# Optimization experiments

Measured on AMD Instinct MI355X. Metric: run time of the kernel, lower is better.

## Reference

```python
import jax, jax.numpy as jnp
import numpy as np
import math

B, S, HID = 2, 2048, 1152
NH, NKV = 16, 4
HD = HID // NH  # 72
GROUPS = NH // NKV  # 4
ROPE_BASE = 10000.0


def setup_inputs() -> dict:
    key = jax.random.key(0)
    ks = jax.random.split(key, 5)
    hidden_states = jax.random.normal(ks[0], (B, S, HID), dtype=jnp.float32)
    # causal additive mask: 0 on/below diagonal, -1e9 above
    causal = jnp.tril(jnp.ones((S, S), dtype=jnp.bool_))
    attention_mask = jnp.where(causal, 0.0, -1e9).astype(jnp.float32)[None, None]
    scale = 0.02
    wq = jax.random.normal(ks[1], (HID, HID), dtype=jnp.float32) * scale
    wk = jax.random.normal(ks[2], (NKV * HD, HID), dtype=jnp.float32) * scale
    wv = jax.random.normal(ks[3], (NKV * HD, HID), dtype=jnp.float32) * scale
    wo = jax.random.normal(ks[4], (HID, HID), dtype=jnp.float32) * scale
    return {"hidden_states": hidden_states, "attention_mask": attention_mask,
            "wq": wq, "wk": wk, "wv": wv, "wo": wo}


def _rotate_half(x):
    x1, x2 = jnp.split(x, 2, axis=-1)
    return jnp.concatenate((-x2, x1), axis=-1)


def _rope_cos_sin(seq_len, dim, dtype):
    inv_freq = 1.0 / (ROPE_BASE ** (jnp.arange(0, dim, 2, dtype=jnp.float32) / dim))
    t = jnp.arange(seq_len, dtype=jnp.float32)
    freqs = jnp.outer(t, inv_freq)          # [S, dim/2]
    emb = jnp.concatenate((freqs, freqs), axis=-1)  # [S, dim]
    return jnp.cos(emb).astype(dtype), jnp.sin(emb).astype(dtype)


def reference(hidden_states, attention_mask, wq, wk, wv, wo):
    b, s, _ = hidden_states.shape
    # projections (nn.Linear: x @ W.T)
    q = (hidden_states @ wq.T).reshape(b, s, NH, HD).transpose(0, 2, 1, 3)    # [b,nh,s,hd]
    k = (hidden_states @ wk.T).reshape(b, s, NKV, HD).transpose(0, 2, 1, 3)   # [b,nkv,s,hd]
    v = (hidden_states @ wv.T).reshape(b, s, NKV, HD).transpose(0, 2, 1, 3)
    # RoPE
    cos, sin = _rope_cos_sin(s, HD, hidden_states.dtype)
    cos, sin = cos[None, None], sin[None, None]  # [1,1,s,hd]
    q = q * cos + _rotate_half(q) * sin
    k = k * cos + _rotate_half(k) * sin
    # expand kv heads (repeat_interleave over head dim)
    k = jnp.repeat(k, GROUPS, axis=1)  # [b,nh,s,hd]
    v = jnp.repeat(v, GROUPS, axis=1)
    scores = jnp.einsum('bhqd,bhkd->bhqk', q, k) / math.sqrt(HD)
    scores = scores + attention_mask
    attn = jax.nn.softmax(scores.astype(jnp.float32), axis=-1).astype(q.dtype)
    out = jnp.einsum('bhqk,bhkd->bhqd', attn, v)
    out = out.transpose(0, 2, 1, 3).reshape(b, s, HID)
    return out @ wo.T
```

## Files before the change

### kernel.cpp

```cpp
#include <hip/hip_runtime.h>
#include <hip/hip_bf16.h>
#include <cstddef>

#define B_   2
#define S_   2048
#define HID_ 1152
#define NH_  16
#define NKV_ 4
#define HD_  72
#define MTOT (B_ * S_)
#define KVDIM (NKV_ * HD_)

typedef float f32x4 __attribute__((ext_vector_type(4)));
typedef short bf16x8 __attribute__((ext_vector_type(8)));
typedef short s4v __attribute__((ext_vector_type(4)));

__device__ __forceinline__ float bf2f(short x) {
  unsigned int u = ((unsigned int)(unsigned short)x) << 16;
  return __builtin_bit_cast(float, u);
}
__device__ __forceinline__ short f2bf(float f) {
  unsigned int u = __builtin_bit_cast(unsigned int, f);
  u += 0x7fff + ((u >> 16) & 1);
  return (short)(u >> 16);
}

__device__ __forceinline__ float fast_exp2(float x) {
#if __has_builtin(__builtin_amdgcn_exp2f)
  return __builtin_amdgcn_exp2f(x);
#else
  return exp2f(x);
#endif
}

__device__ __forceinline__ void async16(const short* g, short* lds) {
  __builtin_amdgcn_global_load_lds((const __attribute__((address_space(1))) void*)g,
                                   (__attribute__((address_space(3))) void*)lds,
                                   16, 0, 0);
}

__global__ void k_cvt_all(const float4* __restrict__ s0, const float4* __restrict__ s1,
                          const float4* __restrict__ s2, const float4* __restrict__ s3,
                          const float4* __restrict__ s4,
                          s4v* __restrict__ d0, s4v* __restrict__ d1, s4v* __restrict__ d2,
                          s4v* __restrict__ d3, s4v* __restrict__ d4,
                          float2* __restrict__ tab,
                          int n0, int n1, int n2, int n3, int n4t) {
  int ncvt = n0 + n1 + n2 + n3 + n4t;
  int total = ncvt + S_ * 36;
  for (int i = blockIdx.x * blockDim.x + threadIdx.x; i < total;
       i += gridDim.x * blockDim.x) {
    if (i < ncvt) {
      const float4* s;
      s4v* d;
      int off = i;
      if (off < n0) { s = s0; d = d0; }
      else {
        off -= n0;
        if (off < n1) { s = s1; d = d1; }
        else {
          off -= n1;
          if (off < n2) { s = s2; d = d2; }
          else {
            off -= n2;
            if (off < n3) { s = s3; d = d3; }
            else { off -= n3; s = s4; d = d4; }
          }
        }
      }
      float4 v = s[off];
      s4v o = { f2bf(v.x), f2bf(v.y), f2bf(v.z), f2bf(v.w) };
      d[off] = o;
    } else {
      int idx = i - ncvt;
      int ii = idx % 36, s = idx / 36;
      float freq = powf(10000.0f, -(float)ii / 36.0f);
      float a = (float)s * freq;
      tab[idx] = make_float2(cosf(a), sinf(a));
    }
  }
}

__global__ void k_post(short* __restrict__ Qb, short* __restrict__ Kb,
                       const short* __restrict__ Vb, short* __restrict__ Vt,
                       const float2* __restrict__ tab) {
  int idx = blockIdx.x * blockDim.x + threadIdx.x;
  const int nrope = MTOT * 20 * 36;
  if (idx < nrope) {
    int i = idx % 36;
    int t = idx / 36;
    int hh = t % 20;
    int m = t / 20;
    int s = m & (S_ - 1);
    float2 cs = tab[s * 36 + i];
    short* p = (hh < 16) ? Qb + (size_t)m * HID_ + hh * HD_
                         : Kb + (size_t)m * KVDIM + (hh - 16) * HD_;
    float x1 = bf2f(p[i]), x2 = bf2f(p[i + 36]);
    p[i]      = f2bf(x1 * cs.x - x2 * cs.y);
    p[i + 36] = f2bf(x2 * cs.x + x1 * cs.y);
  } else {
    idx -= nrope;
    if (idx >= 8 * 80 * S_) return;
    int s = idx & (S_ - 1);
    int t2 = idx >> 11;
    int d = t2 % 80;
    int bkv = t2 / 80;
    int b = bkv >> 2, kv = bkv & 3;
    short v = 0;
    if (d < HD_) v = Vb[((size_t)(b * S_ + s)) * KVDIM + kv * HD_ + d];
    else if (d == HD_) v = (short)0x3F80;
    Vt[idx] = v;
  }
}

#define BM 128
#define BN 128
#define BK 32

__global__ __launch_bounds__(256) void k_gemm_qkv(const short* __restrict__ A,
                                                  const short* __restrict__ Wq,
                                                  const short* __restrict__ Wk,
                                                  const short* __restrict__ Wv,
                                                  short* __restrict__ Qo,
                                                  short* __restrict__ Ko,
                                                  short* __restrict__ Vo) {
  const int K = HID_, NTOT = 1728;
  __shared__ short As[BM * BK];
  __shared__ short Bs[BN * BK];
  const int tid = threadIdx.x;
  const int l = tid & 63;
  const int w = tid >> 6;
  const int bm = blockIdx.x * BM;
  const int bn = blockIdx.y * BN;
  const int wr = (w >> 1) * 64;
  const int wc = (w & 1) * 64;
  const int c15 = l & 15, g = l >> 4;
  const int r0 = tid >> 2;
  const int c0 = (tid & 3) * 8;

  f32x4 acc[4][4] = {};

  for (int k0 = 0; k0 < K; k0 += BK) {
#pragma unroll
    for (int it = 0; it < 2; ++it) {
      int ar = bm + it * 64 + r0;
      int br = bn + it * 64 + r0;
      if (br > NTOT - 1) br = NTOT - 1;
      const short* bsrc;
      if (br < 1152)      bsrc = Wq + (size_t)br * K;
      else if (br < 1440) bsrc = Wk + (size_t)(br - 1152) * K;
      else                bsrc = Wv + (size_t)(br - 1440) * K;
      async16(A + (size_t)ar * K + k0 + c0, &As[(it * 64 + r0) * BK + c0]);
      async16(bsrc + k0 + c0, &Bs[(it * 64 + r0) * BK + c0]);
    }
    __syncthreads();
    bf16x8 af[4], bfr[4];
#pragma unroll
    for (int t = 0; t < 4; ++t) {
      af[t]  = *(const bf16x8*)&As[(wr + t * 16 + c15) * BK + g * 8];
      bfr[t] = *(const bf16x8*)&Bs[(wc + t * 16 + c15) * BK + g * 8];
    }
#pragma unroll
    for (int mt = 0; mt < 4; ++mt)
#pragma unroll
      for (int nt = 0; nt < 4; ++nt)
        acc[mt][nt] = __builtin_amdgcn_mfma_f32_16x16x32_bf16(af[mt], bfr[nt], acc[mt][nt], 0, 0, 0);
    __syncthreads();
  }

#pragma unroll
  for (int mt = 0; mt < 4; ++mt)
#pragma unroll
    for (int nt = 0; nt < 4; ++nt)
#pragma unroll
      for (int j = 0; j < 4; ++j) {
        int row = bm + wr + mt * 16 + g * 4 + j;
        int col = bn + wc + nt * 16 + c15;
        short val = f2bf(acc[mt][nt][j]);
        if (col < 1152)      Qo[(size_t)row * HID_ + col] = val;
        else if (col < 1440) Ko[(size_t)row * KVDIM + col - 1152] = val;
        else if (col < NTOT) Vo[(size_t)row * KVDIM + col - 1440] = val;
      }
}

__global__ __launch_bounds__(256) void k_gemm_o(const short* __restrict__ A,
                                                const short* __restrict__ Bm,
                                                float* __restrict__ C,
                                                int M, int N, int K) {
  __shared__ short As[BM * BK];
  __shared__ short Bs[BN * BK];
  const int tid = threadIdx.x;
  const int l = tid & 63;
  const int w = tid >> 6;
  const int bm = blockIdx.x * BM;
  const int bn = blockIdx.y * BN;
  const int wr = (w >> 1) * 64;
  const int wc = (w & 1) * 64;
  const int c15 = l & 15, g = l >> 4;
  const int r0 = tid >> 2;
  const int c0 = (tid & 3) * 8;

  f32x4 acc[4][4] = {};

  for (int k0 = 0; k0 < K; k0 += BK) {
#pragma unroll
    for (int it = 0; it < 2; ++it) {
      int ar = bm + it * 64 + r0;
      int br = bn + it * 64 + r0;
      if (br > N - 1) br = N - 1;
      async16(A + (size_t)ar * K + k0 + c0, &As[(it * 64 + r0) * BK + c0]);
      async16(Bm + (size_t)br * K + k0 + c0, &Bs[(it * 64 + r0) * BK + c0]);
    }
    __syncthreads();
    bf16x8 af[4], bfr[4];
#pragma unroll
    for (int t = 0; t < 4; ++t) {
      af[t]  = *(const bf16x8*)&As[(wr + t * 16 + c15) * BK + g * 8];
      bfr[t] = *(const bf16x8*)&Bs[(wc + t * 16 + c15) * BK + g * 8];
    }
#pragma unroll
    for (int mt = 0; mt < 4; ++mt)
#pragma unroll
      for (int nt = 0; nt < 4; ++nt)
        acc[mt][nt] = __builtin_amdgcn_mfma_f32_16x16x32_bf16(af[mt], bfr[nt], acc[mt][nt], 0, 0, 0);
    __syncthreads();
  }

#pragma unroll
  for (int mt = 0; mt < 4; ++mt)
#pragma unroll
    for (int nt = 0; nt < 4; ++nt)
#pragma unroll
      for (int j = 0; j < 4; ++j) {
        int row = bm + wr + mt * 16 + g * 4 + j;
        int col = bn + wc + nt * 16 + c15;
        if (col < N) C[(size_t)row * N + col] = acc[mt][nt][j];
      }
}

#define QB 16
#define KT 64

__global__ __launch_bounds__(256, 2) void k_flash(const short* __restrict__ Q,
                                                  const short* __restrict__ Kg,
                                                  const short* __restrict__ Vt,
                                                  short* __restrict__ O) {
  const int bid = blockIdx.x;
  const int bkv = bid & 7;
  const int qt = 127 - (bid >> 3);
  const int b = bkv >> 2, kv = bkv & 3;
  const int tid = threadIdx.x;
  const int w = tid >> 6, l = tid & 63;
  const int h = kv * 4 + w;
  const int q0 = qt * QB;
  const int c15 = l & 15, g = l >> 4;

  __shared__ short lds[24064];
  short* Ks0 = lds;
  short* Ks1 = lds + 9728;
  short* Ps  = lds + 19456 + w * 1152;

  const float SCL = 0.117851130f * 1.4426950408889634f;
  const float SHIFT = 8.0f;

  const short* Qbase = Q + (size_t)(b * S_) * HID_ + h * HD_;
  const short* Kbase = Kg + (size_t)(b * S_) * KVDIM + kv * HD_;
  const short* Vbase = Vt + (size_t)bkv * 80 * S_;

  const short* gk[3];
  const short* gv[3];
  int lk[3], lv[3];
  bool vkf[3], vvf[3];
#pragma unroll
  for (int i = 0; i < 3; ++i) {
    int c = tid + 256 * i;
    vkf[i] = c < 576;
    int row = c / 9, cc = c - row * 9;
    if (row > 63) row = 63;
    gk[i] = Kbase + (size_t)row * KVDIM + cc * 8;
    lk[i] = c < 576 ? c * 8 : 0;
    int c2 = tid + 256 * i;
    vvf[i] = c2 < 640;
    int vrow = (c2 >> 3) & 127, slot = c2 & 7;
    if (vrow > 79) vrow = 79;
    gv[i] = Vbase + (size_t)vrow * S_ + ((slot ^ (vrow & 7)) << 3);
    lv[i] = c2 < 640 ? c2 * 8 : 0;
  }

  const int lane_k = c15 * 72 + g * 8;
  const short* rKa = Ks0 + lane_k;
  const short* rKb = Ks1 + lane_k;
  const int lane_v0 = 4608 + c15 * 64 + ((g ^ (c15 & 7)) << 3);
  const int lane_v1 = 4608 + c15 * 64 + (((4 + g) ^ (c15 & 7)) << 3);
  const short* rV0a = lds + lane_v0;
  const short* rV0b = lds + 9728 + lane_v0;
  const short* rV1a = lds + lane_v1;
  const short* rV1b = lds + 9728 + lane_v1;
  short* pPw = Ps + g * 288 + c15;
  const short* pPr = Ps + c15 * 72 + g * 8;

  bf16x8 qf[3];
  const bf16x8 zfrag = {0, 0, 0, 0, 0, 0, 0, 0};
  {
    int row = q0 + c15;
#pragma unroll
    for (int ks = 0; ks < 3; ++ks) {
      int d0 = ks * 32 + g * 8;
      qf[ks] = (d0 < HD_) ? *(const bf16x8*)(Qbase + (size_t)row * HID_ + d0) : zfrag;
    }
#pragma unroll
    for (int ks = 0; ks < 3; ++ks)
#pragma unroll
      for (int e = 0; e < 8; ++e)
        qf[ks][e] = f2bf(bf2f(qf[ks][e]) * SCL);
  }

  f32x4 accO[5] = {};

  const int nkt = (q0 + QB + KT - 1) / KT;
  const int nfull = (QB * qt + 1) >> 6;

  auto STAGE = [&](short* Kd, short* Vd) {
#pragma unroll
    for (int i = 0; i < 3; ++i) {
      if (vkf[i]) async16(gk[i], Kd + lk[i]);
      if (vvf[i]) async16(gv[i], Vd + lv[i]);
      gk[i] += KT * KVDIM;
      gv[i] += KT;
    }
  };

  STAGE(Ks0, lds + 4608);
  const short *rKc = rKa, *rKn = rKb;
  const short *rV0c = rV0a, *rV0n = rV0b;
  const short *rV1c = rV1a, *rV1n = rV1b;
  short *sKn = Ks1, *sVn = lds + 14336;
  short *sKc = Ks0, *sVc = lds + 4608;

  for (int kt = 0; kt < nkt; ++kt) {
    asm volatile("s_waitcnt vmcnt(0)" ::: "memory");
    __builtin_amdgcn_sched_barrier(0);
    __syncthreads();
    if (kt + 1 < nkt) STAGE(sKn, sVn);

    const int kbase = kt * KT;

    f32x4 sc[4] = {};
    __builtin_amdgcn_s_setprio(1);
#pragma unroll
    for (int ct = 0; ct < 4; ++ct)
#pragma unroll
      for (int ks = 0; ks < 3; ++ks) {
        bf16x8 kf = *(const bf16x8*)&rKc[ct * 1152 + ks * 32];
        sc[ct] = __builtin_amdgcn_mfma_f32_16x16x32_bf16(qf[ks], kf, sc[ct], 0, 0, 0);
      }
    __builtin_amdgcn_s_setprio(0);

    const int qrow = q0 + g * 4;
    if (kt >= nfull) {
#pragma unroll
      for (int ct = 0; ct < 4; ++ct) {
        int col = kbase + ct * 16 + c15;
#pragma unroll
        for (int j = 0; j < 4; ++j)
          if (col > qrow + j) sc[ct][j] = -1e30f;
      }
    }
#pragma unroll
    for (int ct = 0; ct < 4; ++ct)
#pragma unroll
      for (int j = 0; j < 4; ++j)
        sc[ct][j] = fast_exp2(sc[ct][j] - SHIFT);

#pragma unroll
    for (int ct = 0; ct < 4; ++ct)
#pragma unroll
      for (int j = 0; j < 4; ++j)
        pPw[j * 72 + ct * 16] = f2bf(sc[ct][j]);
    asm volatile("s_waitcnt lgkmcnt(0)" ::: "memory");
    __builtin_amdgcn_sched_barrier(0);
    bf16x8 pa0 = *(const bf16x8*)&pPr[0];
    bf16x8 pa1 = *(const bf16x8*)&pPr[32];

    __builtin_amdgcn_s_setprio(1);
#pragma unroll
    for (int dt = 0; dt < 5; ++dt) {
      bf16x8 vb0 = *(const bf16x8*)&rV0c[dt * 1024];
      bf16x8 vb1 = *(const bf16x8*)&rV1c[dt * 1024];
      accO[dt] = __builtin_amdgcn_mfma_f32_16x16x32_bf16(pa0, vb0, accO[dt], 0, 0, 0);
      accO[dt] = __builtin_amdgcn_mfma_f32_16x16x32_bf16(pa1, vb1, accO[dt], 0, 0, 0);
    }
    __builtin_amdgcn_s_setprio(0);

    const short* t;
    t = rKc; rKc = rKn; rKn = t;
    t = rV0c; rV0c = rV0n; rV0n = t;
    t = rV1c; rV1c = rV1n; rV1n = t;
    short* ts;
    ts = sKc; sKc = sKn; sKn = ts;
    ts = sVc; sVc = sVn; sVn = ts;
  }

  float lj[4];
#pragma unroll
  for (int j = 0; j < 4; ++j)
    lj[j] = 1.0f / __shfl(accO[4][j], (l & 48) | 8);
#pragma unroll
  for (int dt = 0; dt < 5; ++dt) {
    int d = dt * 16 + c15;
    if (d < HD_) {
#pragma unroll
      for (int j = 0; j < 4; ++j) {
        int row = q0 + g * 4 + j;
        O[(size_t)(b * S_ + row) * HID_ + h * HD_ + d] = f2bf(accO[dt][j] * lj[j]);
      }
    }
  }
}

extern "C" void kernel_launch(void* const* d_in, const int* in_sizes, int n_in,
                              void* d_out, int out_size, void* d_ws, size_t ws_size,
                              hipStream_t stream) {
  const float* hs = (const float*)d_in[0];
  const float* wq = (const float*)d_in[2];
  const float* wk = (const float*)d_in[3];
  const float* wv = (const float*)d_in[4];
  const float* wo = (const float*)d_in[5];

  char* ws = (char*)d_ws;
  short* Xb  = (short*)(ws + 0);
  short* Qb  = (short*)(ws + 9437184);
  short* Kb  = (short*)(ws + 18874368);
  short* Vb  = (short*)(ws + 21233664);
  short* Vt  = (short*)(ws + 23592960);
  short* Ob  = (short*)(ws + 26214400);
  short* wqb = (short*)(ws + 35651584);
  short* wkb = (short*)(ws + 38305792);
  short* wvb = (short*)(ws + 38969344);
  short* wob = (short*)(ws + 39632896);
  float2* tab = (float2*)(ws + 42287104);

  k_cvt_all<<<2048, 256, 0, stream>>>(
      (const float4*)hs, (const float4*)wq, (const float4*)wk, (const float4*)wv,
      (const float4*)wo,
      (s4v*)Xb, (s4v*)wqb, (s4v*)wkb, (s4v*)wvb, (s4v*)wob, tab,
      MTOT * HID_ / 4, HID_ * HID_ / 4, KVDIM * HID_ / 4, KVDIM * HID_ / 4,
      HID_ * HID_ / 4);

  k_gemm_qkv<<<dim3(32, 14), 256, 0, stream>>>(Xb, wqb, wkb, wvb, Qb, Kb, Vb);

  {
    int total = MTOT * 20 * 36 + 8 * 80 * S_;
    k_post<<<(total + 255) / 256, 256, 0, stream>>>(Qb, Kb, Vb, Vt, tab);
  }

  k_flash<<<1024, 256, 0, stream>>>(Qb, Kb, Vt, Ob);

  k_gemm_o<<<dim3(32, 9), 256, 0, stream>>>(Ob, wob, (float*)d_out, MTOT, HID_, HID_);
}
```

Measured before the change: 133.4 us.

## Fuse RoPE and V transpose into QKV GEMM epilogue and flash Q load

```diff
diff --git a/kernel.cpp b/kernel.cpp
--- a/kernel.cpp
+++ b/kernel.cpp
@@ -44,23 +44,25 @@
                           const float4* __restrict__ s4,
                           s4v* __restrict__ d0, s4v* __restrict__ d1, s4v* __restrict__ d2,
                           s4v* __restrict__ d3, s4v* __restrict__ d4,
-                          float2* __restrict__ tab,
+                          float2* __restrict__ tab, short* __restrict__ Vt,
                           int n0, int n1, int n2, int n3, int n4t) {
   int ncvt = n0 + n1 + n2 + n3 + n4t;
-  int total = ncvt + S_ * 36;
+  int ntab = S_ * 36;
+  int total = ncvt + ntab + 32768;
   for (int i = blockIdx.x * blockDim.x + threadIdx.x; i < total;
        i += gridDim.x * blockDim.x) {
     if (i < ncvt) {
       const float4* s;
       s4v* d;
       int off = i;
+      bool perm = false;
       if (off < n0) { s = s0; d = d0; }
       else {
         off -= n0;
-        if (off < n1) { s = s1; d = d1; }
+        if (off < n1) { s = s1; d = d1; perm = true; }
         else {
           off -= n1;
-          if (off < n2) { s = s2; d = d2; }
+          if (off < n2) { s = s2; d = d2; perm = true; }
           else {
             off -= n2;
             if (off < n3) { s = s3; d = d3; }
@@ -70,46 +72,32 @@
       }
       float4 v = s[off];
       s4v o = { f2bf(v.x), f2bf(v.y), f2bf(v.z), f2bf(v.w) };
-      d[off] = o;
-    } else {
+      int out = off;
+      if (perm) {
+        int r = off / 288, k4 = off - r * 288;
+        int hh = r / 72, ii = r - hh * 72;
+        int pr = hh * 72 + (ii < 36 ? 2 * ii : 2 * (ii - 36) + 1);
+        out = pr * 288 + k4;
+      }
+      d[out] = o;
+    } else if (i < ncvt + ntab) {
       int idx = i - ncvt;
       int ii = idx % 36, s = idx / 36;
       float freq = powf(10000.0f, -(float)ii / 36.0f);
       float a = (float)s * freq;
       tab[idx] = make_float2(cosf(a), sinf(a));
-    }
-  }
-}
-
-__global__ void k_post(short* __restrict__ Qb, short* __restrict__ Kb,
-                       const short* __restrict__ Vb, short* __restrict__ Vt,
-                       const float2* __restrict__ tab) {
-  int idx = blockIdx.x * blockDim.x + threadIdx.x;
-  const int nrope = MTOT * 20 * 36;
-  if (idx < nrope) {
-    int i = idx % 36;
-    int t = idx / 36;
-    int hh = t % 20;
-    int m = t / 20;
-    int s = m & (S_ - 1);
-    float2 cs = tab[s * 36 + i];
-    short* p = (hh < 16) ? Qb + (size_t)m * HID_ + hh * HD_
-                         : Kb + (size_t)m * KVDIM + (hh - 16) * HD_;
-    float x1 = bf2f(p[i]), x2 = bf2f(p[i + 36]);
-    p[i]      = f2bf(x1 * cs.x - x2 * cs.y);
-    p[i + 36] = f2bf(x2 * cs.x + x1 * cs.y);
-  } else {
-    idx -= nrope;
-    if (idx >= 8 * 80 * S_) return;
-    int s = idx & (S_ - 1);
-    int t2 = idx >> 11;
-    int d = t2 % 80;
-    int bkv = t2 / 80;
-    int b = bkv >> 2, kv = bkv & 3;
-    short v = 0;
-    if (d < HD_) v = Vb[((size_t)(b * S_ + s)) * KVDIM + kv * HD_ + d];
-    else if (d == HD_) v = (short)0x3F80;
-    Vt[idx] = v;
+    } else {
+      int idx2 = i - ncvt - ntab;
+      int t = idx2 << 2;
+      int sp = t & 2047;
+      int rest = t >> 11;
+      int dr = rest & 7;
+      int bkv = rest >> 3;
+      s4v val = {};
+      if (dr == 0) { val[0] = (short)0x3F80; val[1] = (short)0x3F80;
+                     val[2] = (short)0x3F80; val[3] = (short)0x3F80; }
+      *(s4v*)(Vt + (size_t)bkv * 163840 + (size_t)(72 + dr) * 2048 + sp) = val;
+    }
   }
 }
 
@@ -123,7 +111,8 @@
                                                   const short* __restrict__ Wv,
                                                   short* __restrict__ Qo,
                                                   short* __restrict__ Ko,
-                                                  short* __restrict__ Vo) {
+                                                  short* __restrict__ Vt,
+                                                  const float2* __restrict__ tab) {
   const int K = HID_, NTOT = 1728;
   __shared__ short As[BM * BK];
   __shared__ short Bs[BN * BK];
@@ -171,16 +160,38 @@
 #pragma unroll
   for (int mt = 0; mt < 4; ++mt)
 #pragma unroll
-    for (int nt = 0; nt < 4; ++nt)
-#pragma unroll
-      for (int j = 0; j < 4; ++j) {
-        int row = bm + wr + mt * 16 + g * 4 + j;
-        int col = bn + wc + nt * 16 + c15;
-        short val = f2bf(acc[mt][nt][j]);
-        if (col < 1152)      Qo[(size_t)row * HID_ + col] = val;
-        else if (col < 1440) Ko[(size_t)row * KVDIM + col - 1152] = val;
-        else if (col < NTOT) Vo[(size_t)row * KVDIM + col - 1440] = val;
-      }
+    for (int nt = 0; nt < 4; ++nt) {
+      int col = bn + wc + nt * 16 + c15;
+      if (col < 1152) {
+#pragma unroll
+        for (int j = 0; j < 4; ++j) {
+          int row = bm + wr + mt * 16 + g * 4 + j;
+          Qo[(size_t)row * HID_ + col] = f2bf(acc[mt][nt][j]);
+        }
+      } else if (col < 1440) {
+        int ch = col - 1152;
+        int ii = (ch % 72) >> 1;
+#pragma unroll
+        for (int j = 0; j < 4; ++j) {
+          int row = bm + wr + mt * 16 + g * 4 + j;
+          float v = acc[mt][nt][j];
+          float p = __shfl_xor(v, 1);
+          float2 cs = tab[(size_t)(row & (S_ - 1)) * 36 + ii];
+          float r = (c15 & 1) ? (v * cs.x + p * cs.y)
+                              : (v * cs.x - p * cs.y);
+          Ko[(size_t)row * KVDIM + ch] = f2bf(r);
+        }
+      } else if (col < NTOT) {
+        int cv = col - 1440;
+        int d = cv % 72, kvh = cv / 72;
+        int row0 = bm + wr + mt * 16 + g * 4;
+        int bkv = (row0 >> 11) * 4 + kvh;
+        s4v out;
+#pragma unroll
+        for (int j = 0; j < 4; ++j) out[j] = f2bf(acc[mt][nt][j]);
+        *(s4v*)(Vt + (size_t)bkv * 163840 + (size_t)d * 2048 + (row0 & 2047)) = out;
+      }
+    }
 }
 
 __global__ __launch_bounds__(256) void k_gemm_o(const short* __restrict__ A,
@@ -244,7 +255,8 @@
 __global__ __launch_bounds__(256, 2) void k_flash(const short* __restrict__ Q,
                                                   const short* __restrict__ Kg,
                                                   const short* __restrict__ Vt,
-                                                  short* __restrict__ O) {
+                                                  short* __restrict__ O,
+                                                  const float2* __restrict__ tab) {
   const int bid = blockIdx.x;
   const int bkv = bid & 7;
   const int qt = 127 - (bid >> 3);
@@ -303,16 +315,26 @@
   const bf16x8 zfrag = {0, 0, 0, 0, 0, 0, 0, 0};
   {
     int row = q0 + c15;
+    const short* qrow = Qbase + (size_t)row * HID_;
+    const float2* trow = tab + (size_t)row * 36;
 #pragma unroll
     for (int ks = 0; ks < 3; ++ks) {
       int d0 = ks * 32 + g * 8;
-      qf[ks] = (d0 < HD_) ? *(const bf16x8*)(Qbase + (size_t)row * HID_ + d0) : zfrag;
-    }
-#pragma unroll
-    for (int ks = 0; ks < 3; ++ks)
-#pragma unroll
-      for (int e = 0; e < 8; ++e)
-        qf[ks][e] = f2bf(bf2f(qf[ks][e]) * SCL);
+      if (d0 < HD_) {
+        bf16x8 raw = *(const bf16x8*)(qrow + d0);
+        bf16x8 o;
+#pragma unroll
+        for (int e = 0; e < 8; e += 2) {
+          float2 cs = trow[(d0 + e) >> 1];
+          float x1 = bf2f(raw[e]), x2 = bf2f(raw[e + 1]);
+          o[e]     = f2bf((x1 * cs.x - x2 * cs.y) * SCL);
+          o[e + 1] = f2bf((x2 * cs.x + x1 * cs.y) * SCL);
+        }
+        qf[ks] = o;
+      } else {
+        qf[ks] = zfrag;
+      }
+    }
   }
 
   f32x4 accO[5] = {};
@@ -431,7 +453,6 @@
   short* Xb  = (short*)(ws + 0);
   short* Qb  = (short*)(ws + 9437184);
   short* Kb  = (short*)(ws + 18874368);
-  short* Vb  = (short*)(ws + 21233664);
   short* Vt  = (short*)(ws + 23592960);
   short* Ob  = (short*)(ws + 26214400);
   short* wqb = (short*)(ws + 35651584);
@@ -443,18 +464,13 @@
   k_cvt_all<<<2048, 256, 0, stream>>>(
       (const float4*)hs, (const float4*)wq, (const float4*)wk, (const float4*)wv,
       (const float4*)wo,
-      (s4v*)Xb, (s4v*)wqb, (s4v*)wkb, (s4v*)wvb, (s4v*)wob, tab,
+      (s4v*)Xb, (s4v*)wqb, (s4v*)wkb, (s4v*)wvb, (s4v*)wob, tab, Vt,
       MTOT * HID_ / 4, HID_ * HID_ / 4, KVDIM * HID_ / 4, KVDIM * HID_ / 4,
       HID_ * HID_ / 4);
 
-  k_gemm_qkv<<<dim3(32, 14), 256, 0, stream>>>(Xb, wqb, wkb, wvb, Qb, Kb, Vb);
-
-  {
-    int total = MTOT * 20 * 36 + 8 * 80 * S_;
-    k_post<<<(total + 255) / 256, 256, 0, stream>>>(Qb, Kb, Vb, Vt, tab);
-  }
-
-  k_flash<<<1024, 256, 0, stream>>>(Qb, Kb, Vt, Ob);
+  k_gemm_qkv<<<dim3(32, 14), 256, 0, stream>>>(Xb, wqb, wkb, wvb, Qb, Kb, Vt, tab);
+
+  k_flash<<<1024, 256, 0, stream>>>(Qb, Kb, Vt, Ob, tab);
 
   k_gemm_o<<<dim3(32, 9), 256, 0, stream>>>(Ob, wob, (float*)d_out, MTOT, HID_, HID_);
 }
```

After: 123.9 us. -7.1%, faster.
